# Performance work log

Hardware: AMD Instinct MI355X
Metric: run time of the kernel (lower is better)

The kernel has to match this reference:

```python
import jax, jax.numpy as jnp
import numpy as np

TEMP = 0.07
GTEMP = 1.0

def _l2n(x):
    # tf.nn.l2_normalize with default axis=None: GLOBAL normalization (matches original code)
    return x * jax.lax.rsqrt(jnp.maximum(jnp.sum(x * x), 1e-12))

def _gumbel(key, shape):
    u = jax.random.uniform(key, shape, minval=1e-20, maxval=1.0)
    return -jnp.log(-jnp.log(u))

def _gumbel_softmax(key, logits, temp, hard):
    y = jax.nn.softmax((logits + _gumbel(key, logits.shape)) / temp, axis=-1)
    if hard:
        y_hard = jax.nn.one_hot(jnp.argmax(y, axis=-1), logits.shape[-1], dtype=y.dtype)
        y = y_hard + y - jax.lax.stop_gradient(y)  # straight-through
    return y

def _cross_rep(key, feat, context):
    # feat: [B, D], context: [K, D]
    k1, k2, k3 = jax.random.split(key, 3)
    kn = context @ feat.T                       # [K, B] codebook similarity
    logits = kn.T                               # [B, K]
    assign_n = _gumbel_softmax(k1, logits, GTEMP, False)   # soft assignment [B, K]
    hard_n = _gumbel_softmax(k2, logits, GTEMP, True)      # hard assignment [B, K]
    agg_n = _l2n(assign_n @ context)            # [B, D]
    # stochastic binary threshold on the K->B heat map
    eps = jax.random.uniform(k3, kn.shape)      # uniform(-0.5,0.5)*1 + 0.5 == U(0,1)
    prob = jax.nn.sigmoid(kn)
    binary = (prob > eps).astype(feat.dtype)
    assign_k = binary + prob - jax.lax.stop_gradient(prob)  # straight-through binary
    agg_k = assign_k @ feat                      # [K, D]
    agg_k = agg_k / (jnp.sum(assign_k, axis=1, keepdims=True) + 1e-8)
    agg_k = _l2n(agg_k)
    assignment = jnp.argmax(hard_n, axis=1)      # [B]
    return assignment, agg_n, agg_k

def _info_nce(q, kpos, negs, temp):
    l_pos = jnp.sum(q * kpos, axis=1, keepdims=True)   # [N, 1]
    l_neg = q @ negs.T                                  # [N, L]
    logits = jnp.concatenate([l_pos, l_neg], axis=1) / temp
    # cross-entropy with label 0 (positive in first column)
    return jnp.mean(jax.nn.logsumexp(logits, axis=1) - logits[:, 0])

def reference(feat_1, feat_2, context_1, context_2, queue_n, queue_k):
    key = jax.random.key(42)
    kq, kc1, kc2 = jax.random.split(key, 3)
    qn = jax.lax.stop_gradient(_l2n(queue_n))
    qk = jax.lax.stop_gradient(_l2n(queue_k))
    assign_1, agg_n_1, agg_k_1 = _cross_rep(kc1, feat_1, context_1)
    assign_2, agg_n_2, agg_k_2 = _cross_rep(kc2, feat_2, context_2)
    loss_n = _info_nce(agg_n_1, agg_n_2, qn, TEMP)
    queue = jax.lax.stop_gradient(qk + 0.1 * jax.random.normal(kq, qk.shape) + qk)
    queue = _l2n(queue)
    loss_k = _info_nce(agg_k_1, jax.lax.stop_gradient(agg_k_2), queue, TEMP)
    loss = loss_n + loss_k
    return assign_1, agg_n_2, agg_k_2, loss

def setup_inputs() -> dict:
    key = jax.random.key(0)
    k1, k2, k3, k4, k5, k6 = jax.random.split(key, 6)
    B, D, K, L, Q = 4096, 256, 512, 32768, 8192
    return {
        'feat_1': jax.random.normal(k1, (B, D), dtype=jnp.float32),
        'feat_2': jax.random.normal(k2, (B, D), dtype=jnp.float32),
        'context_1': jax.random.normal(k3, (K, D), dtype=jnp.float32) * 0.05,
        'context_2': jax.random.normal(k4, (K, D), dtype=jnp.float32) * 0.05,
        'queue_n': jax.random.normal(k5, (L, D), dtype=jnp.float32),
        'queue_k': jax.random.normal(k6, (Q, D), dtype=jnp.float32),
    }
```

## Files before the change

kernel.cpp:

```cpp
#include <hip/hip_runtime.h>
#include <stdint.h>
#include <math.h>

typedef unsigned int u32;

#define BB 4096
#define DD 256
#define KK 512
#define LL 32768
#define QQ 8192

__host__ __device__ inline void tf2x32(u32 k0, u32 k1, u32 c0, u32 c1, u32& o0, u32& o1) {
  u32 ks2 = k0 ^ k1 ^ 0x1BD11BDAu;
  u32 x0 = c0 + k0, x1 = c1 + k1;
#define TF_R(r) { x0 += x1; x1 = ((x1 << (r)) | (x1 >> (32 - (r)))); x1 ^= x0; }
  TF_R(13) TF_R(15) TF_R(26) TF_R(6)
  x0 += k1; x1 += ks2 + 1u;
  TF_R(17) TF_R(29) TF_R(16) TF_R(24)
  x0 += ks2; x1 += k0 + 2u;
  TF_R(13) TF_R(15) TF_R(26) TF_R(6)
  x0 += k0; x1 += k1 + 3u;
  TF_R(17) TF_R(29) TF_R(16) TF_R(24)
  x0 += k1; x1 += ks2 + 4u;
  TF_R(13) TF_R(15) TF_R(26) TF_R(6)
  x0 += ks2; x1 += k0 + 5u;
#undef TF_R
  o0 = x0; o1 = x1;
}

__device__ inline u32 rbits32(u32 k0, u32 k1, u32 i) {
  u32 a, b;
  tf2x32(k0, k1, 0u, i, a, b);
  return a ^ b;
}

__device__ inline float u01f(u32 bits) {
  return __uint_as_float(0x3f800000u | (bits >> 9)) - 1.0f;
}

__device__ inline float gumbel_at(u32 k0, u32 k1, u32 i) {
  float f = u01f(rbits32(k0, k1, i));
  float u = fmaxf(1e-20f, f + 1e-20f);
  float l1 = (float)log((double)u);
  float l2 = (float)log((double)(-l1));
  return -l2;
}

__device__ inline float gumbel_f32(u32 k0, u32 k1, u32 i) {
  float f = u01f(rbits32(k0, k1, i));
  float u = fmaxf(1e-20f, f + 1e-20f);
  float l1 = __logf(u);
  return -__logf(-l1);
}

__device__ inline float erfinv32(float x) {
  float w = -log1pf(-x * x);
  float p;
  if (w < 5.0f) {
    w -= 2.5f;
    p = 2.81022636e-08f;
    p = fmaf(p, w, 3.43273939e-07f);
    p = fmaf(p, w, -3.5233877e-06f);
    p = fmaf(p, w, -4.39150654e-06f);
    p = fmaf(p, w, 0.00021858087f);
    p = fmaf(p, w, -0.00125372503f);
    p = fmaf(p, w, -0.00417768164f);
    p = fmaf(p, w, 0.246640727f);
    p = fmaf(p, w, 1.50140941f);
  } else {
    w = sqrtf(w) - 3.0f;
    p = -0.000200214257f;
    p = fmaf(p, w, 0.000100950558f);
    p = fmaf(p, w, 0.00134934322f);
    p = fmaf(p, w, -0.00367342844f);
    p = fmaf(p, w, 0.00573950773f);
    p = fmaf(p, w, -0.0076224613f);
    p = fmaf(p, w, 0.00943887047f);
    p = fmaf(p, w, 1.00167406f);
    p = fmaf(p, w, 2.83297682f);
  }
  return p * x;
}

__global__ __launch_bounds__(256)
void k_sumsq(const float* __restrict__ x, int n, float* __restrict__ partial) {
  __shared__ float sm[256];
  float s = 0.0f;
  for (int i = blockIdx.x * 256 + threadIdx.x; i < n; i += gridDim.x * 256) {
    float v = x[i]; s = fmaf(v, v, s);
  }
  sm[threadIdx.x] = s; __syncthreads();
  for (int off = 128; off > 0; off >>= 1) {
    if (threadIdx.x < off) sm[threadIdx.x] += sm[threadIdx.x + off];
    __syncthreads();
  }
  if (threadIdx.x == 0) partial[blockIdx.x] = sm[0];
}

__global__ __launch_bounds__(256)
void k_stats(const float* __restrict__ qn, const float* __restrict__ qk_in,
             const float* __restrict__ partK,
             float* __restrict__ colpart, float* __restrict__ sqpart,
             u32 kqa, u32 kqb) {
  __shared__ float smc[4][256];
  __shared__ float sm[256];
  int tid = threadIdx.x, g = tid >> 6, l = tid & 63;
  int z = blockIdx.y;
  float4 ca = {0.f, 0.f, 0.f, 0.f};
  float ss = 0.0f;
  if (z == 0) {
    int base = blockIdx.x * 64;
    for (int j = base + g; j < base + 64; j += 4) {
      float4 v = *(const float4*)(qn + (size_t)j * 256 + l * 4);
      ca.x += v.x; ca.y += v.y; ca.z += v.z; ca.w += v.w;
      ss = fmaf(v.x, v.x, ss); ss = fmaf(v.y, v.y, ss);
      ss = fmaf(v.z, v.z, ss); ss = fmaf(v.w, v.w, ss);
    }
  } else {
    sm[tid] = partK[tid]; __syncthreads();
    for (int off = 128; off > 0; off >>= 1) {
      if (tid < off) sm[tid] += sm[tid + off];
      __syncthreads();
    }
    float sk = (float)(1.0 / sqrt((double)fmaxf(sm[0], 1e-12f)));
    __syncthreads();
    const float lo = -0.99999994f;
    int base = blockIdx.x * 16;
    for (int j = base + g; j < base + 16; j += 4) {
      int i0 = j * 256 + l * 4;
      float4 v = *(const float4*)(qk_in + i0);
      float vin[4] = {v.x, v.y, v.z, v.w};
      float valv[4];
#pragma unroll
      for (int e = 0; e < 4; e++) {
        float qk = vin[e] * sk;
        float f = u01f(rbits32(kqa, kqb, (u32)(i0 + e)));
        float u = fmaxf(lo, f * 2.0f + lo);
        float nv = 1.41421354f * erfinv32(u);
        float t = qk + 0.1f * nv;
        valv[e] = t + qk;
        ss = fmaf(valv[e], valv[e], ss);
      }
      ca.x += valv[0]; ca.y += valv[1]; ca.z += valv[2]; ca.w += valv[3];
    }
  }
  smc[g][l * 4 + 0] = ca.x; smc[g][l * 4 + 1] = ca.y;
  smc[g][l * 4 + 2] = ca.z; smc[g][l * 4 + 3] = ca.w;
  sm[tid] = ss; __syncthreads();
  colpart[(size_t)z * 131072 + blockIdx.x * 256 + tid] =
      (smc[0][tid] + smc[1][tid]) + (smc[2][tid] + smc[3][tid]);
  for (int off = 128; off > 0; off >>= 1) {
    if (tid < off) sm[tid] += sm[tid + off];
    __syncthreads();
  }
  if (tid == 0) sqpart[z * 512 + blockIdx.x] = sm[0];
}

__global__ __launch_bounds__(256)
void k_finalize(const float* __restrict__ colpart, const float* __restrict__ sqpart,
                float* __restrict__ csum, float* __restrict__ lscOut) {
  __shared__ float sm[256];
  int z = blockIdx.y, t = threadIdx.x;
  if (blockIdx.x < 256) {
    int d = blockIdx.x;
    const float* cp = colpart + (size_t)z * 131072;
    float a = cp[(size_t)t * 256 + d] + cp[(size_t)(t + 256) * 256 + d];
    sm[t] = a; __syncthreads();
    for (int off = 128; off > 0; off >>= 1) {
      if (t < off) sm[t] += sm[t + off];
      __syncthreads();
    }
    if (t == 0) csum[z * 256 + d] = sm[0];
  } else {
    const float* sq = sqpart + z * 512;
    float a = sq[t] + sq[t + 256];
    sm[t] = a; __syncthreads();
    for (int off = 128; off > 0; off >>= 1) {
      if (t < off) sm[t] += sm[t + off];
      __syncthreads();
    }
    if (t == 0) {
      float sr = (float)(1.0 / sqrt((double)fmaxf(sm[0], 1e-12f)));
      lscOut[z] = sr / 0.07f;
    }
  }
}

__global__ __launch_bounds__(256)
void k_gemm_nt(const float* __restrict__ A0, const float* __restrict__ A1,
               const float* __restrict__ B0, const float* __restrict__ B1,
               float* __restrict__ C, float* __restrict__ BIN,
               u32 k3a0, u32 k3b0, u32 k3a1, u32 k3b1) {
  __shared__ float As[16][68], Bs[16][68];
  __shared__ float Ts[64][65];
  int tid = threadIdx.x;
  int tx = tid & 15, ty = tid >> 4;
  int rowBase = blockIdx.y * 64, colBase = blockIdx.x * 64;
  int br = blockIdx.z;
  const float* A = br ? A1 : A0;
  const float* Bm = br ? B1 : B0;
  u32 k3a = br ? k3a1 : k3a0, k3b = br ? k3b1 : k3b0;
  float* Cd = C + (size_t)br * BB * KK;
  float* Bd = BIN + (size_t)br * KK * BB;
  float c[4][4] = {};
  for (int kt = 0; kt < 256; kt += 16) {
#pragma unroll
    for (int q = 0; q < 4; q++) {
      int idx = tid + 256 * q;
      int kkx = idx & 15, rr = idx >> 4;
      As[kkx][rr] = A[(size_t)(rowBase + rr) * 256 + kt + kkx];
      Bs[kkx][rr] = Bm[(size_t)(colBase + rr) * 256 + kt + kkx];
    }
    __syncthreads();
#pragma unroll
    for (int kx = 0; kx < 16; kx++) {
      float4 a4 = *(const float4*)&As[kx][ty * 4];
      float4 b4 = *(const float4*)&Bs[kx][tx * 4];
      float av[4] = {a4.x, a4.y, a4.z, a4.w};
      float bv[4] = {b4.x, b4.y, b4.z, b4.w};
#pragma unroll
      for (int r = 0; r < 4; r++)
#pragma unroll
        for (int q = 0; q < 4; q++)
          c[r][q] = fmaf(av[r], bv[q], c[r][q]);
    }
    __syncthreads();
  }
#pragma unroll
  for (int r = 0; r < 4; r++)
#pragma unroll
    for (int q = 0; q < 4; q++) {
      Cd[(size_t)(rowBase + ty * 4 + r) * KK + colBase + tx * 4 + q] = c[r][q];
      Ts[ty * 4 + r][tx * 4 + q] = c[r][q];
    }
  __syncthreads();
#pragma unroll
  for (int p = 0; p < 16; p++) {
    int idx = p * 256 + tid;
    int kl = idx >> 6, bl = idx & 63;
    float x = Ts[bl][kl];
    float prob = 1.0f / (1.0f + expf(-x));
    int k = colBase + kl, b = rowBase + bl;
    u32 i = (u32)(k * BB + b);
    float eps = u01f(rbits32(k3a, k3b, i));
    Bd[(size_t)k * BB + b] = (prob > eps) ? 1.0f : 0.0f;
  }
}

__global__ __launch_bounds__(256)
void k_gemm_aggn(const float* __restrict__ Yb, const float* __restrict__ B0,
                 const float* __restrict__ B1, float* __restrict__ CPN) {
  __shared__ float As[16][68], Bs[16][68];
  int tid = threadIdx.x;
  int tx = tid & 15, ty = tid >> 4;
  int rowBase = blockIdx.y * 64, colBase = blockIdx.x * 64;
  int br = blockIdx.z >> 1, s = blockIdx.z & 1;
  const float* A = Yb + (size_t)br * BB * KK;
  const float* Bm = br ? B1 : B0;
  int k0 = s * 256;
  float c[4][4] = {};
  for (int kt = k0; kt < k0 + 256; kt += 16) {
#pragma unroll
    for (int q = 0; q < 4; q++) {
      int idx = tid + 256 * q;
      int kkx = idx & 15, rr = idx >> 4;
      As[kkx][rr] = A[(size_t)(rowBase + rr) * KK + kt + kkx];
      int kk = (tid >> 6) * 4 + q;
      int jj = tid & 63;
      Bs[kk][jj] = Bm[(size_t)(kt + kk) * DD + colBase + jj];
    }
    __syncthreads();
#pragma unroll
    for (int kx = 0; kx < 16; kx++) {
      float4 a4 = *(const float4*)&As[kx][ty * 4];
      float4 b4 = *(const float4*)&Bs[kx][tx * 4];
      float av[4] = {a4.x, a4.y, a4.z, a4.w};
      float bv[4] = {b4.x, b4.y, b4.z, b4.w};
#pragma unroll
      for (int r = 0; r < 4; r++)
#pragma unroll
        for (int q = 0; q < 4; q++)
          c[r][q] = fmaf(av[r], bv[q], c[r][q]);
    }
    __syncthreads();
  }
  float* dst = CPN + (size_t)blockIdx.z * BB * DD;
#pragma unroll
  for (int r = 0; r < 4; r++)
#pragma unroll
    for (int q = 0; q < 4; q++)
      dst[(size_t)(rowBase + ty * 4 + r) * DD + colBase + tx * 4 + q] = c[r][q];
}

__global__ __launch_bounds__(256)
void k_gemm_aggk(const float* __restrict__ BIN, const float* __restrict__ B0,
                 const float* __restrict__ B1, float* __restrict__ CP) {
  __shared__ float As[16][68], Bs[16][68];
  int tid = threadIdx.x;
  int tx = tid & 15, ty = tid >> 4;
  int rowBase = blockIdx.y * 64, colBase = blockIdx.x * 64;
  int br = blockIdx.z >> 4, s = blockIdx.z & 15;
  const float* A = BIN + (size_t)br * KK * BB;
  const float* Bm = br ? B1 : B0;
  int k0 = s * 256;
  float c[4][4] = {};
  for (int kt = k0; kt < k0 + 256; kt += 16) {
#pragma unroll
    for (int q = 0; q < 4; q++) {
      int idx = tid + 256 * q;
      int kkx = idx & 15, rr = idx >> 4;
      As[kkx][rr] = A[(size_t)(rowBase + rr) * BB + kt + kkx];
      int kk = (tid >> 6) * 4 + q;
      int jj = tid & 63;
      Bs[kk][jj] = Bm[(size_t)(kt + kk) * DD + colBase + jj];
    }
    __syncthreads();
#pragma unroll
    for (int kx = 0; kx < 16; kx++) {
      float4 a4 = *(const float4*)&As[kx][ty * 4];
      float4 b4 = *(const float4*)&Bs[kx][tx * 4];
      float av[4] = {a4.x, a4.y, a4.z, a4.w};
      float bv[4] = {b4.x, b4.y, b4.z, b4.w};
#pragma unroll
      for (int r = 0; r < 4; r++)
#pragma unroll
        for (int q = 0; q < 4; q++)
          c[r][q] = fmaf(av[r], bv[q], c[r][q]);
    }
    __syncthreads();
  }
  float* dst = CP + (size_t)blockIdx.z * KK * DD;
#pragma unroll
  for (int r = 0; r < 4; r++)
#pragma unroll
    for (int q = 0; q < 4; q++)
      dst[(size_t)(rowBase + ty * 4 + r) * DD + colBase + tx * 4 + q] = c[r][q];
}

__global__ __launch_bounds__(256)
void k_reduce(const float* __restrict__ CPN, const float* __restrict__ CP,
              const float* __restrict__ rs2,
              float* __restrict__ N0, float* __restrict__ N1,
              float* __restrict__ K0, float* __restrict__ K1,
              float* __restrict__ sqpN, float* __restrict__ sqpK) {
  __shared__ float sq[256];
  int tid = threadIdx.x, br = blockIdx.y;
  float v;
  if (blockIdx.x < 4096) {
    int i = blockIdx.x * 256 + tid;
    const int MN = BB * DD;
    v = CPN[(size_t)(2 * br) * MN + i] + CPN[(size_t)(2 * br + 1) * MN + i];
    (br ? N1 : N0)[i] = v;
  } else {
    int i = (blockIdx.x - 4096) * 256 + tid;
    const int MN = KK * DD;
    const float* cp = CP + (size_t)br * 16 * MN;
    float s = 0.0f;
    for (int t = 0; t < 16; t++) s += cp[(size_t)t * MN + i];
    v = s / (rs2[br * KK + (i >> 8)] + 1e-8f);
    (br ? K1 : K0)[i] = v;
  }
  sq[tid] = v * v; __syncthreads();
  for (int off = 128; off > 0; off >>= 1) {
    if (tid < off) sq[tid] += sq[tid + off];
    __syncthreads();
  }
  if (tid == 0) {
    if (blockIdx.x < 4096) sqpN[br * 4096 + blockIdx.x] = sq[0];
    else sqpK[br * 512 + (blockIdx.x - 4096)] = sq[0];
  }
}

__global__ __launch_bounds__(256)
void k_scale(float* __restrict__ N0, float* __restrict__ N1,
             float* __restrict__ K0, float* __restrict__ K1,
             const float* __restrict__ sqpN, const float* __restrict__ sqpK) {
  __shared__ float sm[256];
  int tid = threadIdx.x, br = blockIdx.y;
  int isK = (blockIdx.x >= 1024);
  const float* sq = isK ? (sqpK + br * 512) : (sqpN + br * 4096);
  int np = isK ? 512 : 4096;
  float a = 0.0f;
  for (int i = tid; i < np; i += 256) a += sq[i];
  sm[tid] = a; __syncthreads();
  for (int off = 128; off > 0; off >>= 1) {
    if (tid < off) sm[tid] += sm[tid + off];
    __syncthreads();
  }
  float f = (float)(1.0 / sqrt((double)fmaxf(sm[0], 1e-12f)));
  float* data = isK ? (br ? K1 : K0) : (br ? N1 : N0);
  int xb = isK ? (blockIdx.x - 1024) : blockIdx.x;
  int i = (xb * 256 + tid) * 4;
  float4 v = *(const float4*)(data + i);
  v.x *= f; v.y *= f; v.z *= f; v.w *= f;
  *(float4*)(data + i) = v;
}

__global__ __launch_bounds__(256)
void k_softmax_assign(const float* __restrict__ T, float* __restrict__ Y,
                      float* __restrict__ assignOut,
                      u32 g1a0, u32 g1b0, u32 g1a1, u32 g1b1, u32 g2a, u32 g2b) {
  __shared__ float smA[4], smS[4], smM2[4], smS2[4], smV[4], smV2[4];
  __shared__ int smI[4];
  int bid = blockIdx.x, tid = threadIdx.x;
  int br = bid >> 12, b = bid & 4095;
  u32 g1a = br ? g1a1 : g1a0, g1b = br ? g1b1 : g1b0;
  const float* knT = T + (size_t)br * BB * KK;
  float* Yd = Y + (size_t)br * BB * KK;
  int lane = tid & 63, wid = tid >> 6;
  int i0 = b * KK + tid, i1 = i0 + 256;
  float x0 = knT[i0], x1 = knT[i1];

  float z0 = x0 + gumbel_f32(g1a, g1b, (u32)i0);
  float z1 = x1 + gumbel_f32(g1a, g1b, (u32)i1);
  float wm = fmaxf(z0, z1);
#pragma unroll
  for (int off = 1; off < 64; off <<= 1) wm = fmaxf(wm, __shfl_xor(wm, off, 64));
  if (lane == 0) smA[wid] = wm;
  __syncthreads();
  float m = fmaxf(fmaxf(smA[0], smA[1]), fmaxf(smA[2], smA[3]));
  float e0 = expf(z0 - m), e1 = expf(z1 - m);
  float ws = e0 + e1;
#pragma unroll
  for (int off = 1; off < 64; off <<= 1) ws += __shfl_xor(ws, off, 64);
  if (lane == 0) smS[wid] = ws;
  __syncthreads();
  float s = (smS[0] + smS[1]) + (smS[2] + smS[3]);
  Yd[i0] = e0 / s;
  Yd[i1] = e1 / s;

  if (br == 0) {
    float wf0 = x0 + gumbel_f32(g2a, g2b, (u32)i0);
    float wf1 = x1 + gumbel_f32(g2a, g2b, (u32)i1);
    float v1, v2; int i1x;
    if (wf0 >= wf1) { v1 = wf0; i1x = tid; v2 = wf1; }
    else            { v1 = wf1; i1x = tid + 256; v2 = wf0; }
#pragma unroll
    for (int off = 1; off < 64; off <<= 1) {
      float ov1 = __shfl_xor(v1, off, 64);
      int   oi1 = __shfl_xor(i1x, off, 64);
      float ov2 = __shfl_xor(v2, off, 64);
      float n1; int ni;
      if (ov1 > v1 || (ov1 == v1 && oi1 < i1x)) { n1 = ov1; ni = oi1; v2 = fmaxf(v1, ov2); }
      else { n1 = v1; ni = i1x; v2 = fmaxf(v2, ov1 == v1 ? ov2 : ov1); }
      if (ov1 == v1 && oi1 != i1x) v2 = fmaxf(v2, ov1);
      v1 = n1; i1x = ni;
    }
    if (lane == 0) { smV[wid] = v1; smI[wid] = i1x; smV2[wid] = v2; }
    __syncthreads();
    __shared__ int needSlow;
    if (tid == 0) {
      float cv = smV[0]; int ci = smI[0]; float c2 = smV2[0];
#pragma unroll
      for (int t = 1; t < 4; t++) {
        float tv = smV[t]; int ti = smI[t]; float t2 = smV2[t];
        if (tv > cv || (tv == cv && ti < ci)) { c2 = fmaxf(cv, t2); cv = tv; ci = ti; }
        else c2 = fmaxf(c2, tv);
      }
      if (cv - c2 > 5e-5f) { assignOut[b] = (float)ci; needSlow = 0; }
      else needSlow = 1;
    }
    __syncthreads();
    if (needSlow) {
      float w0 = x0 + gumbel_at(g2a, g2b, (u32)i0);
      float w1 = x1 + gumbel_at(g2a, g2b, (u32)i1);
      float wm2 = fmaxf(w0, w1);
#pragma unroll
      for (int off = 1; off < 64; off <<= 1) wm2 = fmaxf(wm2, __shfl_xor(wm2, off, 64));
      if (lane == 0) smM2[wid] = wm2;
      __syncthreads();
      float m2 = fmaxf(fmaxf(smM2[0], smM2[1]), fmaxf(smM2[2], smM2[3]));
      float f0 = expf(w0 - m2), f1 = expf(w1 - m2);
      float ws2 = f0 + f1;
#pragma unroll
      for (int off = 1; off < 64; off <<= 1) ws2 += __shfl_xor(ws2, off, 64);
      if (lane == 0) smS2[wid] = ws2;
      __syncthreads();
      float s2 = (smS2[0] + smS2[1]) + (smS2[2] + smS2[3]);
      float y0 = f0 / s2, y1v = f1 / s2;
      float bv; int bi;
      if (y1v > y0) { bv = y1v; bi = tid + 256; } else { bv = y0; bi = tid; }
#pragma unroll
      for (int off = 1; off < 64; off <<= 1) {
        float ov = __shfl_xor(bv, off, 64);
        int oi = __shfl_xor(bi, off, 64);
        if (ov > bv || (ov == bv && oi < bi)) { bv = ov; bi = oi; }
      }
      if (lane == 0) { smV[wid] = bv; smI[wid] = bi; }
      __syncthreads();
      if (tid == 0) {
        float cv = smV[0]; int ci = smI[0];
#pragma unroll
        for (int t = 1; t < 4; t++) {
          if (smV[t] > cv || (smV[t] == cv && smI[t] < ci)) { cv = smV[t]; ci = smI[t]; }
        }
        assignOut[b] = (float)ci;
      }
    }
  }
}

__global__ __launch_bounds__(256)
void k_rowsum(const float* __restrict__ BIN, float* __restrict__ rs2) {
  __shared__ float sm[4];
  int row = blockIdx.x;
  const float* src = BIN + (size_t)row * BB;
  int tid = threadIdx.x, l = tid & 63, w = tid >> 6;
  float s = 0.0f;
#pragma unroll
  for (int p = 0; p < 4; p++) {
    float4 v = *(const float4*)(src + (p * 256 + tid) * 4);
    s += (v.x + v.y) + (v.z + v.w);
  }
#pragma unroll
  for (int off = 1; off < 64; off <<= 1) s += __shfl_xor(s, off, 64);
  if (l == 0) sm[w] = s;
  __syncthreads();
  if (tid == 0) rs2[row] = (sm[0] + sm[1]) + (sm[2] + sm[3]);
}

__global__ __launch_bounds__(256)
void k_loss_row(const float* __restrict__ QN, const float* __restrict__ KPN,
                const float* __restrict__ QK, const float* __restrict__ KPK,
                const float* __restrict__ csum, const float* __restrict__ lscp,
                float* __restrict__ LPN, float* __restrict__ LPK) {
  __shared__ float pt[4];
  int w = threadIdx.x >> 6, l = threadIdx.x & 63;
  int bid = blockIdx.x;
  int isK = (bid >= 1024);
  int rb = isK ? (bid - 1024) : bid;
  const float* Q  = isK ? QK : QN;
  const float* KP = isK ? KPK : KPN;
  const float* cs4 = csum + (isK ? 256 : 0);
  float Lc = isK ? (float)QQ : (float)LL;
  float lsc = lscp[isK ? 1 : 0];
  int r = rb * 4 + w;
  float4 q = *(const float4*)(Q + (size_t)r * 256 + l * 4);
  float4 kp = *(const float4*)(KP + (size_t)r * 256 + l * 4);
  float4 cs = *(const float4*)(cs4 + l * 4);
  float d1 = q.x * kp.x + q.y * kp.y + q.z * kp.z + q.w * kp.w;
  float d2 = q.x * cs.x + q.y * cs.y + q.z * cs.z + q.w * cs.w;
#pragma unroll
  for (int off = 1; off < 64; off <<= 1) {
    d1 += __shfl_xor(d1, off, 64);
    d2 += __shfl_xor(d2, off, 64);
  }
  if (l == 0) {
    float z0 = d1 / 0.07f;
    double S = (double)Lc + (double)expf(z0) + (double)(lsc * d2);
    pt[w] = (float)(log(S)) - z0;
  }
  __syncthreads();
  if (threadIdx.x == 0) {
    float v = (pt[0] + pt[1]) + (pt[2] + pt[3]);
    if (isK) LPK[rb] = v; else LPN[rb] = v;
  }
}

__global__ __launch_bounds__(256)
void k_loss_final(const float* __restrict__ LPN, int nN, float invMN,
                  const float* __restrict__ LPK, int nK, float invMK,
                  float* __restrict__ outLoss) {
  __shared__ float sm[256];
  int tid = threadIdx.x;
  float a = 0.0f;
  for (int i = tid; i < nN; i += 256) a += LPN[i];
  sm[tid] = a; __syncthreads();
  for (int off = 128; off > 0; off >>= 1) {
    if (tid < off) sm[tid] += sm[tid + off];
    __syncthreads();
  }
  float lossN = sm[0] * invMN;
  __syncthreads();
  float b = 0.0f;
  for (int i = tid; i < nK; i += 256) b += LPK[i];
  sm[tid] = b; __syncthreads();
  for (int off = 128; off > 0; off >>= 1) {
    if (tid < off) sm[tid] += sm[tid + off];
    __syncthreads();
  }
  if (tid == 0) outLoss[0] = lossN + sm[0] * invMK;
}

extern "C" void kernel_launch(void* const* d_in, const int* in_sizes, int n_in,
                              void* d_out, int out_size, void* d_ws, size_t ws_size,
                              hipStream_t stream) {
  const float* feat0 = (const float*)d_in[0];
  const float* feat1 = (const float*)d_in[1];
  const float* ctx0  = (const float*)d_in[2];
  const float* ctx1  = (const float*)d_in[3];
  const float* queue_n = (const float*)d_in[4];
  const float* queue_k = (const float*)d_in[5];

  float* W = (float*)d_ws;
  size_t o = 0;
  float* T     = W + o; o += 2 * (size_t)BB * KK;
  float* Yb    = W + o; o += 2 * (size_t)BB * KK;
  float* BIN   = W + o; o += 2 * (size_t)KK * BB;
  float* CP    = W + o; o += 32 * (size_t)KK * DD;
  float* CPN   = W + o; o += 4 * (size_t)BB * DD;
  float* AGGN1 = W + o; o += (size_t)BB * DD;
  float* AGGK1 = W + o; o += (size_t)KK * DD;
  float* RS2   = W + o; o += 2 * KK;
  float* CPS   = W + o; o += 2 * 131072;
  float* SQ2   = W + o; o += 2 * 512;
  float* CS    = W + o; o += 2 * 256;
  float* LSC   = W + o; o += 2;
  float* LPN   = W + o; o += 1024;
  float* LPK   = W + o; o += 128;
  float* PART_K = W + o; o += 256;
  float* SQPN  = W + o; o += 2 * 4096;
  float* SQPK  = W + o; o += 2 * 512;

  float* out = (float*)d_out;
  float* outAssign = out;
  float* outAggn2  = out + BB;
  float* outAggk2  = out + BB + (size_t)BB * DD;
  float* outLoss   = out + BB + (size_t)BB * DD + (size_t)KK * DD;

  u32 kq0, kq1, kc[2][2];
  tf2x32(0u, 42u, 0u, 0u, kq0, kq1);
  tf2x32(0u, 42u, 0u, 1u, kc[0][0], kc[0][1]);
  tf2x32(0u, 42u, 0u, 2u, kc[1][0], kc[1][1]);
  u32 sub[2][3][2];
  for (int br = 0; br < 2; br++)
    for (int t = 0; t < 3; t++)
      tf2x32(kc[br][0], kc[br][1], 0u, (u32)t, sub[br][t][0], sub[br][t][1]);

  k_sumsq<<<256, 256, 0, stream>>>(queue_k, QQ * DD, PART_K);
  k_stats<<<dim3(512, 2), 256, 0, stream>>>(queue_n, queue_k, PART_K, CPS, SQ2, kq0, kq1);
  k_finalize<<<dim3(257, 2), 256, 0, stream>>>(CPS, SQ2, CS, LSC);

  k_gemm_nt<<<dim3(KK / 64, BB / 64, 2), 256, 0, stream>>>(
      feat0, feat1, ctx0, ctx1, T, BIN,
      sub[0][2][0], sub[0][2][1], sub[1][2][0], sub[1][2][1]);
  k_softmax_assign<<<2 * BB, 256, 0, stream>>>(T, Yb, outAssign,
      sub[0][0][0], sub[0][0][1], sub[1][0][0], sub[1][0][1], sub[0][1][0], sub[0][1][1]);
  k_rowsum<<<2 * KK, 256, 0, stream>>>(BIN, RS2);
  k_gemm_aggn<<<dim3(DD / 64, BB / 64, 4), 256, 0, stream>>>(Yb, ctx0, ctx1, CPN);
  k_gemm_aggk<<<dim3(DD / 64, KK / 64, 32), 256, 0, stream>>>(BIN, feat0, feat1, CP);
  k_reduce<<<dim3(4608, 2), 256, 0, stream>>>(CPN, CP, RS2, AGGN1, outAggn2,
                                              AGGK1, outAggk2, SQPN, SQPK);
  k_scale<<<dim3(1152, 2), 256, 0, stream>>>(AGGN1, outAggn2, AGGK1, outAggk2, SQPN, SQPK);

  k_loss_row<<<1152, 256, 0, stream>>>(AGGN1, outAggn2, AGGK1, outAggk2, CS, LSC, LPN, LPK);
  k_loss_final<<<1, 256, 0, stream>>>(LPN, BB / 4, 1.0f / BB, LPK, KK / 4, 1.0f / KK, outLoss);
}
```

Before: 208.2 us.

## Move aggregation GEMMs to bf16 MFMA with pre-swizzled packed operands

Result: faster. 176.3 us (-15.3%).

```diff
diff --git a/kernel.cpp b/kernel.cpp
--- a/kernel.cpp
+++ b/kernel.cpp
@@ -3,6 +3,9 @@
 #include <math.h>
 
 typedef unsigned int u32;
+typedef unsigned short u16;
+typedef __attribute__((ext_vector_type(8))) short short8;
+typedef __attribute__((ext_vector_type(4))) float f32x4;
 
 #define BB 4096
 #define DD 256
@@ -82,6 +85,12 @@
   return p * x;
 }
 
+__device__ inline u16 f2bf(float f) {
+  u32 u = __float_as_uint(f);
+  u32 r = (u + 0x7FFFu + ((u >> 16) & 1u)) >> 16;
+  return (u16)r;
+}
+
 __global__ __launch_bounds__(256)
 void k_sumsq(const float* __restrict__ x, int n, float* __restrict__ partial) {
   __shared__ float sm[256];
@@ -187,9 +196,36 @@
 }
 
 __global__ __launch_bounds__(256)
+void k_pack(const float* __restrict__ f0, const float* __restrict__ f1,
+            const float* __restrict__ c0, const float* __restrict__ c1,
+            u16* __restrict__ featP, u16* __restrict__ ctxP) {
+  int idx = blockIdx.x * 256 + threadIdx.x;
+  if (idx < 2 * BB * DD) {
+    int br = idx >> 20;
+    int r = idx & ((1 << 20) - 1);
+    int b = r >> 8, d = r & 255;
+    float v = (br ? f1 : f0)[r];
+    size_t dst = ((size_t)(br * 16 + (d >> 4)) * 128 + (b >> 5)) * 512 +
+                 (((d & 15) | (((b >> 3) & 3) << 4)) * 8) + (b & 7);
+    featP[dst] = f2bf(v);
+  } else {
+    int j = idx - 2 * BB * DD;
+    if (j < 2 * KK * DD) {
+      int br = j >> 17;
+      int r = j & 131071;
+      int k = r >> 8, n = r & 255;
+      float v = (br ? c1 : c0)[r];
+      size_t dst = ((size_t)(br * 16 + (n >> 4)) * 16 + (k >> 5)) * 512 +
+                   (((n & 15) | (((k >> 3) & 3) << 4)) * 8) + (k & 7);
+      ctxP[dst] = f2bf(v);
+    }
+  }
+}
+
+__global__ __launch_bounds__(256)
 void k_gemm_nt(const float* __restrict__ A0, const float* __restrict__ A1,
                const float* __restrict__ B0, const float* __restrict__ B1,
-               float* __restrict__ C, float* __restrict__ BIN,
+               float* __restrict__ C, u16* __restrict__ BINP,
                u32 k3a0, u32 k3b0, u32 k3a1, u32 k3b1) {
   __shared__ float As[16][68], Bs[16][68];
   __shared__ float Ts[64][65];
@@ -201,7 +237,7 @@
   const float* Bm = br ? B1 : B0;
   u32 k3a = br ? k3a1 : k3a0, k3b = br ? k3b1 : k3b0;
   float* Cd = C + (size_t)br * BB * KK;
-  float* Bd = BIN + (size_t)br * KK * BB;
+  u16* Bd = BINP + (size_t)br * 32 * 128 * 512;
   float c[4][4] = {};
   for (int kt = 0; kt < 256; kt += 16) {
 #pragma unroll
@@ -243,98 +279,74 @@
     int k = colBase + kl, b = rowBase + bl;
     u32 i = (u32)(k * BB + b);
     float eps = u01f(rbits32(k3a, k3b, i));
-    Bd[(size_t)k * BB + b] = (prob > eps) ? 1.0f : 0.0f;
-  }
-}
-
-__global__ __launch_bounds__(256)
-void k_gemm_aggn(const float* __restrict__ Yb, const float* __restrict__ B0,
-                 const float* __restrict__ B1, float* __restrict__ CPN) {
-  __shared__ float As[16][68], Bs[16][68];
-  int tid = threadIdx.x;
-  int tx = tid & 15, ty = tid >> 4;
-  int rowBase = blockIdx.y * 64, colBase = blockIdx.x * 64;
-  int br = blockIdx.z >> 1, s = blockIdx.z & 1;
-  const float* A = Yb + (size_t)br * BB * KK;
-  const float* Bm = br ? B1 : B0;
-  int k0 = s * 256;
-  float c[4][4] = {};
-  for (int kt = k0; kt < k0 + 256; kt += 16) {
-#pragma unroll
-    for (int q = 0; q < 4; q++) {
-      int idx = tid + 256 * q;
-      int kkx = idx & 15, rr = idx >> 4;
-      As[kkx][rr] = A[(size_t)(rowBase + rr) * KK + kt + kkx];
-      int kk = (tid >> 6) * 4 + q;
-      int jj = tid & 63;
-      Bs[kk][jj] = Bm[(size_t)(kt + kk) * DD + colBase + jj];
-    }
-    __syncthreads();
-#pragma unroll
-    for (int kx = 0; kx < 16; kx++) {
-      float4 a4 = *(const float4*)&As[kx][ty * 4];
-      float4 b4 = *(const float4*)&Bs[kx][tx * 4];
-      float av[4] = {a4.x, a4.y, a4.z, a4.w};
-      float bv[4] = {b4.x, b4.y, b4.z, b4.w};
-#pragma unroll
-      for (int r = 0; r < 4; r++)
-#pragma unroll
-        for (int q = 0; q < 4; q++)
-          c[r][q] = fmaf(av[r], bv[q], c[r][q]);
-    }
-    __syncthreads();
-  }
-  float* dst = CPN + (size_t)blockIdx.z * BB * DD;
-#pragma unroll
-  for (int r = 0; r < 4; r++)
-#pragma unroll
-    for (int q = 0; q < 4; q++)
-      dst[(size_t)(rowBase + ty * 4 + r) * DD + colBase + tx * 4 + q] = c[r][q];
-}
-
-__global__ __launch_bounds__(256)
-void k_gemm_aggk(const float* __restrict__ BIN, const float* __restrict__ B0,
-                 const float* __restrict__ B1, float* __restrict__ CP) {
-  __shared__ float As[16][68], Bs[16][68];
-  int tid = threadIdx.x;
-  int tx = tid & 15, ty = tid >> 4;
-  int rowBase = blockIdx.y * 64, colBase = blockIdx.x * 64;
-  int br = blockIdx.z >> 4, s = blockIdx.z & 15;
-  const float* A = BIN + (size_t)br * KK * BB;
-  const float* Bm = br ? B1 : B0;
-  int k0 = s * 256;
-  float c[4][4] = {};
-  for (int kt = k0; kt < k0 + 256; kt += 16) {
-#pragma unroll
-    for (int q = 0; q < 4; q++) {
-      int idx = tid + 256 * q;
-      int kkx = idx & 15, rr = idx >> 4;
-      As[kkx][rr] = A[(size_t)(rowBase + rr) * BB + kt + kkx];
-      int kk = (tid >> 6) * 4 + q;
-      int jj = tid & 63;
-      Bs[kk][jj] = Bm[(size_t)(kt + kk) * DD + colBase + jj];
-    }
-    __syncthreads();
-#pragma unroll
-    for (int kx = 0; kx < 16; kx++) {
-      float4 a4 = *(const float4*)&As[kx][ty * 4];
-      float4 b4 = *(const float4*)&Bs[kx][tx * 4];
-      float av[4] = {a4.x, a4.y, a4.z, a4.w};
-      float bv[4] = {b4.x, b4.y, b4.z, b4.w};
-#pragma unroll
-      for (int r = 0; r < 4; r++)
-#pragma unroll
-        for (int q = 0; q < 4; q++)
-          c[r][q] = fmaf(av[r], bv[q], c[r][q]);
-    }
-    __syncthreads();
-  }
-  float* dst = CP + (size_t)blockIdx.z * KK * DD;
-#pragma unroll
-  for (int r = 0; r < 4; r++)
-#pragma unroll
-    for (int q = 0; q < 4; q++)
-      dst[(size_t)(rowBase + ty * 4 + r) * DD + colBase + tx * 4 + q] = c[r][q];
+    size_t bo = ((size_t)(k >> 4) * 128 + (b >> 5)) * 512 +
+                (((k & 15) | (((b >> 3) & 3) << 4)) * 8) + (b & 7);
+    Bd[bo] = (prob > eps) ? (u16)0x3F80 : (u16)0;
+  }
+}
+
+__global__ __launch_bounds__(256)
+void k_mfma_aggn(const u16* __restrict__ YP, const u16* __restrict__ ctxP,
+                 float* __restrict__ CPN) {
+  int gx = blockIdx.x, s = blockIdx.y, br = blockIdx.z;
+  int tid = threadIdx.x, w = tid >> 6, lane = tid & 63;
+  f32x4 acc0 = {0,0,0,0}, acc1 = {0,0,0,0}, acc2 = {0,0,0,0}, acc3 = {0,0,0,0};
+  const u16* Ab = YP + ((size_t)(br * 256 + gx) * 16) * 512 + lane * 8;
+  const u16* Bb = ctxP + ((size_t)(br * 16) * 16) * 512 + lane * 8;
+  for (int kc = 0; kc < 8; kc++) {
+    int kcg = s * 8 + kc;
+    short8 a = *(const short8*)(Ab + (size_t)kcg * 512);
+    short8 b0 = *(const short8*)(Bb + ((size_t)(w * 4 + 0) * 16 + kcg) * 512);
+    short8 b1 = *(const short8*)(Bb + ((size_t)(w * 4 + 1) * 16 + kcg) * 512);
+    short8 b2 = *(const short8*)(Bb + ((size_t)(w * 4 + 2) * 16 + kcg) * 512);
+    short8 b3 = *(const short8*)(Bb + ((size_t)(w * 4 + 3) * 16 + kcg) * 512);
+    acc0 = __builtin_amdgcn_mfma_f32_16x16x32_bf16(a, b0, acc0, 0, 0, 0);
+    acc1 = __builtin_amdgcn_mfma_f32_16x16x32_bf16(a, b1, acc1, 0, 0, 0);
+    acc2 = __builtin_amdgcn_mfma_f32_16x16x32_bf16(a, b2, acc2, 0, 0, 0);
+    acc3 = __builtin_amdgcn_mfma_f32_16x16x32_bf16(a, b3, acc3, 0, 0, 0);
+  }
+  float* dst = CPN + (size_t)(br * 2 + s) * BB * DD;
+  int rbase = gx * 16 + (lane >> 4) * 4;
+  int cl = lane & 15;
+#pragma unroll
+  for (int r = 0; r < 4; r++) {
+    dst[(size_t)(rbase + r) * 256 + (w * 4 + 0) * 16 + cl] = acc0[r];
+    dst[(size_t)(rbase + r) * 256 + (w * 4 + 1) * 16 + cl] = acc1[r];
+    dst[(size_t)(rbase + r) * 256 + (w * 4 + 2) * 16 + cl] = acc2[r];
+    dst[(size_t)(rbase + r) * 256 + (w * 4 + 3) * 16 + cl] = acc3[r];
+  }
+}
+
+__global__ __launch_bounds__(256)
+void k_mfma_aggk(const u16* __restrict__ BINP, const u16* __restrict__ featP,
+                 float* __restrict__ CP) {
+  int gx = blockIdx.x, s = blockIdx.y, br = blockIdx.z;
+  int tid = threadIdx.x, w = tid >> 6, lane = tid & 63;
+  f32x4 acc0 = {0,0,0,0}, acc1 = {0,0,0,0}, acc2 = {0,0,0,0}, acc3 = {0,0,0,0};
+  const u16* Ab = BINP + ((size_t)(br * 32 + gx) * 128) * 512 + lane * 8;
+  const u16* Bb = featP + ((size_t)(br * 16) * 128) * 512 + lane * 8;
+  for (int kc = 0; kc < 8; kc++) {
+    int bcg = s * 8 + kc;
+    short8 a = *(const short8*)(Ab + (size_t)bcg * 512);
+    short8 b0 = *(const short8*)(Bb + ((size_t)(w * 4 + 0) * 128 + bcg) * 512);
+    short8 b1 = *(const short8*)(Bb + ((size_t)(w * 4 + 1) * 128 + bcg) * 512);
+    short8 b2 = *(const short8*)(Bb + ((size_t)(w * 4 + 2) * 128 + bcg) * 512);
+    short8 b3 = *(const short8*)(Bb + ((size_t)(w * 4 + 3) * 128 + bcg) * 512);
+    acc0 = __builtin_amdgcn_mfma_f32_16x16x32_bf16(a, b0, acc0, 0, 0, 0);
+    acc1 = __builtin_amdgcn_mfma_f32_16x16x32_bf16(a, b1, acc1, 0, 0, 0);
+    acc2 = __builtin_amdgcn_mfma_f32_16x16x32_bf16(a, b2, acc2, 0, 0, 0);
+    acc3 = __builtin_amdgcn_mfma_f32_16x16x32_bf16(a, b3, acc3, 0, 0, 0);
+  }
+  float* dst = CP + (size_t)(br * 16 + s) * KK * DD;
+  int rbase = gx * 16 + (lane >> 4) * 4;
+  int cl = lane & 15;
+#pragma unroll
+  for (int r = 0; r < 4; r++) {
+    dst[(size_t)(rbase + r) * 256 + (w * 4 + 0) * 16 + cl] = acc0[r];
+    dst[(size_t)(rbase + r) * 256 + (w * 4 + 1) * 16 + cl] = acc1[r];
+    dst[(size_t)(rbase + r) * 256 + (w * 4 + 2) * 16 + cl] = acc2[r];
+    dst[(size_t)(rbase + r) * 256 + (w * 4 + 3) * 16 + cl] = acc3[r];
+  }
 }
 
 __global__ __launch_bounds__(256)
@@ -397,7 +409,7 @@
 }
 
 __global__ __launch_bounds__(256)
-void k_softmax_assign(const float* __restrict__ T, float* __restrict__ Y,
+void k_softmax_assign(const float* __restrict__ T, u16* __restrict__ YP,
                       float* __restrict__ assignOut,
                       u32 g1a0, u32 g1b0, u32 g1a1, u32 g1b1, u32 g2a, u32 g2b) {
   __shared__ float smA[4], smS[4], smM2[4], smS2[4], smV[4], smV2[4];
@@ -406,7 +418,6 @@
   int br = bid >> 12, b = bid & 4095;
   u32 g1a = br ? g1a1 : g1a0, g1b = br ? g1b1 : g1b0;
   const float* knT = T + (size_t)br * BB * KK;
-  float* Yd = Y + (size_t)br * BB * KK;
   int lane = tid & 63, wid = tid >> 6;
   int i0 = b * KK + tid, i1 = i0 + 256;
   float x0 = knT[i0], x1 = knT[i1];
@@ -426,8 +437,15 @@
   if (lane == 0) smS[wid] = ws;
   __syncthreads();
   float s = (smS[0] + smS[1]) + (smS[2] + smS[3]);
-  Yd[i0] = e0 / s;
-  Yd[i1] = e1 / s;
+  {
+    int k0 = tid, k1 = tid + 256;
+    size_t y0o = ((size_t)(br * 256 + (b >> 4)) * 16 + (k0 >> 5)) * 512 +
+                 ((b & 15) | (((k0 >> 3) & 3) << 4)) * 8 + (k0 & 7);
+    size_t y1o = ((size_t)(br * 256 + (b >> 4)) * 16 + (k1 >> 5)) * 512 +
+                 ((b & 15) | (((k1 >> 3) & 3) << 4)) * 8 + (k1 & 7);
+    YP[y0o] = f2bf(e0 / s);
+    YP[y1o] = f2bf(e1 / s);
+  }
 
   if (br == 0) {
     float wf0 = x0 + gumbel_f32(g2a, g2b, (u32)i0);
@@ -501,22 +519,30 @@
 }
 
 __global__ __launch_bounds__(256)
-void k_rowsum(const float* __restrict__ BIN, float* __restrict__ rs2) {
-  __shared__ float sm[4];
-  int row = blockIdx.x;
-  const float* src = BIN + (size_t)row * BB;
-  int tid = threadIdx.x, l = tid & 63, w = tid >> 6;
-  float s = 0.0f;
-#pragma unroll
-  for (int p = 0; p < 4; p++) {
-    float4 v = *(const float4*)(src + (p * 256 + tid) * 4);
-    s += (v.x + v.y) + (v.z + v.w);
-  }
-#pragma unroll
-  for (int off = 1; off < 64; off <<= 1) s += __shfl_xor(s, off, 64);
-  if (l == 0) sm[w] = s;
-  __syncthreads();
-  if (tid == 0) rs2[row] = (sm[0] + sm[1]) + (sm[2] + sm[3]);
+void k_rowsum(const u16* __restrict__ BINP, float* __restrict__ rs2) {
+  __shared__ int sm[256];
+  int bid = blockIdx.x, br = bid >> 9, k = bid & 511;
+  const u16* base = BINP + ((size_t)(br * 32 + (k >> 4)) * 128) * 512;
+  int klane = k & 15;
+  int tid = threadIdx.x;
+  int cnt = 0;
+#pragma unroll
+  for (int p = 0; p < 2; p++) {
+    int idx = p * 256 + tid;
+    int bc = idx >> 2, hi = idx & 3;
+    const u16* ptr = base + (size_t)bc * 512 + (klane | (hi << 4)) * 8;
+    uint4 v = *(const uint4*)ptr;
+    cnt += (int)((v.x >> 7) & 1) + (int)((v.x >> 23) & 1)
+         + (int)((v.y >> 7) & 1) + (int)((v.y >> 23) & 1)
+         + (int)((v.z >> 7) & 1) + (int)((v.z >> 23) & 1)
+         + (int)((v.w >> 7) & 1) + (int)((v.w >> 23) & 1);
+  }
+  sm[tid] = cnt; __syncthreads();
+  for (int off = 128; off > 0; off >>= 1) {
+    if (tid < off) sm[tid] += sm[tid + off];
+    __syncthreads();
+  }
+  if (tid == 0) rs2[bid] = (float)sm[0];
 }
 
 __global__ __launch_bounds__(256)
@@ -595,8 +621,6 @@
   float* W = (float*)d_ws;
   size_t o = 0;
   float* T     = W + o; o += 2 * (size_t)BB * KK;
-  float* Yb    = W + o; o += 2 * (size_t)BB * KK;
-  float* BIN   = W + o; o += 2 * (size_t)KK * BB;
   float* CP    = W + o; o += 32 * (size_t)KK * DD;
   float* CPN   = W + o; o += 4 * (size_t)BB * DD;
   float* AGGN1 = W + o; o += (size_t)BB * DD;
@@ -611,6 +635,10 @@
   float* PART_K = W + o; o += 256;
   float* SQPN  = W + o; o += 2 * 4096;
   float* SQPK  = W + o; o += 2 * 512;
+  u16* YP    = (u16*)(W + o); o += (size_t)BB * KK;
+  u16* BINP  = (u16*)(W + o); o += (size_t)BB * KK;
+  u16* featP = (u16*)(W + o); o += (size_t)BB * DD;
+  u16* ctxP  = (u16*)(W + o); o += (size_t)KK * DD;
 
   float* out = (float*)d_out;
   float* outAssign = out;
@@ -630,15 +658,17 @@
   k_sumsq<<<256, 256, 0, stream>>>(queue_k, QQ * DD, PART_K);
   k_stats<<<dim3(512, 2), 256, 0, stream>>>(queue_n, queue_k, PART_K, CPS, SQ2, kq0, kq1);
   k_finalize<<<dim3(257, 2), 256, 0, stream>>>(CPS, SQ2, CS, LSC);
+  k_pack<<<(2 * BB * DD + 2 * KK * DD) / 256, 256, 0, stream>>>(
+      feat0, feat1, ctx0, ctx1, featP, ctxP);
 
   k_gemm_nt<<<dim3(KK / 64, BB / 64, 2), 256, 0, stream>>>(
-      feat0, feat1, ctx0, ctx1, T, BIN,
+      feat0, feat1, ctx0, ctx1, T, BINP,
       sub[0][2][0], sub[0][2][1], sub[1][2][0], sub[1][2][1]);
-  k_softmax_assign<<<2 * BB, 256, 0, stream>>>(T, Yb, outAssign,
+  k_softmax_assign<<<2 * BB, 256, 0, stream>>>(T, YP, outAssign,
       sub[0][0][0], sub[0][0][1], sub[1][0][0], sub[1][0][1], sub[0][1][0], sub[0][1][1]);
-  k_rowsum<<<2 * KK, 256, 0, stream>>>(BIN, RS2);
-  k_gemm_aggn<<<dim3(DD / 64, BB / 64, 4), 256, 0, stream>>>(Yb, ctx0, ctx1, CPN);
-  k_gemm_aggk<<<dim3(DD / 64, KK / 64, 32), 256, 0, stream>>>(BIN, feat0, feat1, CP);
+  k_rowsum<<<2 * KK, 256, 0, stream>>>(BINP, RS2);
+  k_mfma_aggn<<<dim3(256, 2, 2), 256, 0, stream>>>(YP, ctxP, CPN);
+  k_mfma_aggk<<<dim3(32, 16, 2), 256, 0, stream>>>(BINP, featP, CP);
   k_reduce<<<dim3(4608, 2), 256, 0, stream>>>(CPN, CP, RS2, AGGN1, outAggn2,
                                               AGGK1, outAggk2, SQPN, SQPK);
   k_scale<<<dim3(1152, 2), 256, 0, stream>>>(AGGN1, outAggn2, AGGK1, outAggk2, SQPN, SQPK);
```
